# Kernel tuning notes

Measured on AMD Instinct MI355X. Metric: run time of the kernel, lower is better.

## Reference

```python
import jax, jax.numpy as jnp
import numpy as np

B, F, D, C, K = 131072, 32, 16, 64, 8  # batch, features, qsvt degree, classes, KAN grid
CLIP = 1.0 - 1e-6


def setup_inputs() -> dict:
    key = jax.random.key(0)
    ks = jax.random.split(key, 7)
    return {
        "X": jax.random.normal(ks[0], (B, F), jnp.float32),
        "qsvt_phases": 0.1 * jax.random.normal(ks[1], (D,), jnp.float32),
        "lcu_weights": jax.random.uniform(ks[2], (F, D), jnp.float32),
        "sum_scale": jnp.ones((F,), jnp.float32) + 0.1 * jax.random.normal(ks[3], (F,), jnp.float32),
        "sum_bias": 0.1 * jax.random.normal(ks[4], (F,), jnp.float32),
        "kan_coeff": jax.random.normal(ks[5], (C, F, K), jnp.float32) / np.sqrt(F * K),
        "kan_bias": jnp.zeros((C,), jnp.float32),
    }


def reference(X, qsvt_phases, lcu_weights, sum_scale, sum_bias, kan_coeff, kan_bias):
    # QSVT: Chebyshev-with-phases polynomial features of each scalar input,
    # vectorized over (batch, feature) instead of the original Python loops.
    degree = qsvt_phases.shape[0]
    grid = kan_coeff.shape[-1]
    theta = jnp.arccos(jnp.clip(X, -CLIP, CLIP))                  # [B,F]
    kd = jnp.arange(1, degree + 1, dtype=X.dtype)                 # [D]
    qsvt_vecs = jnp.cos(theta[..., None] * kd + qsvt_phases)      # [B,F,D]
    # LCU block: normalized linear combination over the degree axis -> scalar per (b,f)
    lcu = jnp.sum(qsvt_vecs * lcu_weights, axis=-1) / (
        jnp.sum(jnp.abs(lcu_weights), axis=-1) + 1e-6)            # [B,F]
    # QuantumSumBlock (one per feature): per-feature affine + tanh squash
    feat = jnp.tanh(sum_scale * lcu + sum_bias)                   # [B,F]
    # KAN layer: Chebyshev basis expansion then per-(class,feature,basis) coefficients
    t2 = jnp.arccos(jnp.clip(feat, -CLIP, CLIP))                  # [B,F]
    kk = jnp.arange(grid, dtype=X.dtype)                          # [K]
    basis = jnp.cos(t2[..., None] * kk)                           # [B,F,K]
    return jnp.einsum('bfk,cfk->bc', basis, kan_coeff) + kan_bias  # [B,C]
```

## Files before the change

### kernel.cpp

```cpp
#include <hip/hip_runtime.h>
#include <hip/hip_bf16.h>

#define F 32
#define Dd 16
#define C 64
#define Kk 8
#define CLIPV (1.0f - 1e-6f)
#define K2 2.8853900817779268f
#define NBLK 1024
#define MT 2

typedef short v8s __attribute__((ext_vector_type(8)));
typedef float v4f __attribute__((ext_vector_type(4)));
typedef float v2f __attribute__((ext_vector_type(2)));

static __device__ inline unsigned pkbf(float lo, float hi) {
    const unsigned l = __bfloat16_as_ushort(__float2bfloat16(lo));
    const unsigned hh = __bfloat16_as_ushort(__float2bfloat16(hi));
    return l | (hh << 16);
}

#define BAR_WRITES() do {                                        \
    asm volatile("s_waitcnt lgkmcnt(0)" ::: "memory");           \
    __builtin_amdgcn_s_barrier();                                \
    asm volatile("" ::: "memory");                               \
} while (0)
#define BAR_READS() do {                                         \
    asm volatile("" ::: "memory");                               \
    __builtin_amdgcn_s_barrier();                                \
    asm volatile("" ::: "memory");                               \
} while (0)

__global__ __launch_bounds__(256, 4) void qkan_kernel(
    const float* __restrict__ X,
    const float* __restrict__ phases,
    const float* __restrict__ lcu_w,
    const float* __restrict__ sscale,
    const float* __restrict__ sbias,
    const float* __restrict__ coeff,
    const float* __restrict__ kbias,
    float* __restrict__ out)
{
    __shared__ unsigned short s_basis[F * 512];

    const int tid = threadIdx.x;
    const int lane = tid & 63;
    const int wu = __builtin_amdgcn_readfirstlane(tid >> 6);
    const int h = lane >> 4;
    const int r16 = lane & 15;
    const int fe = tid & 31;
    const int fe7 = fe & 7;
    const int rg = tid >> 5;

    const int rb0 = blockIdx.x * (MT * 64);

    float xq[8];
    {
        const float* xp = X + (size_t)(rb0 + rg * 8) * F + fe;
#pragma unroll
        for (int m = 0; m < 8; ++m) xq[m] = __builtin_nontemporal_load(xp + m * F);
    }

    float sp0, cp0;
    __sincosf(phases[lane & 15], &sp0, &cp0);

    v2f cc[16];
    float fbias;
    {
        const float* lwf = lcu_w + fe * Dd;
        float wv[16];
        float asum = 0.f;
#pragma unroll
        for (int d = 0; d < Dd; ++d) {
            wv[d] = lwf[d];
            asum += fabsf(wv[d]);
        }
        const float sc = K2 * sscale[fe] / (asum + 1e-6f);
#pragma unroll
        for (int d = 0; d < Dd; ++d) {
            const float cpd = __shfl(cp0, d, 16);
            const float spd = __shfl(sp0, d, 16);
            cc[d][0] = sc * wv[d] * cpd;
            cc[d][1] = -sc * wv[d] * spd;
        }
        fbias = K2 * sbias[fe];
    }

    v8s Bfr[8];
    const int cidx = wu * 16 + r16;
#pragma unroll
    for (int q = 0; q < 8; ++q) {
        const float* gp = coeff + ((size_t)(cidx * F + 4 * q + h) * Kk);
        const float4 g0 = *reinterpret_cast<const float4*>(gp);
        const float4 g1 = *reinterpret_cast<const float4*>(gp + 4);
        union { unsigned u[4]; v8s v; } bb;
        bb.u[0] = pkbf(g0.x, g0.y);
        bb.u[1] = pkbf(g0.z, g0.w);
        bb.u[2] = pkbf(g1.x, g1.y);
        bb.u[3] = pkbf(g1.z, g1.w);
        Bfr[q] = bb.v;
    }
    const float biasreg = kbias[cidx];

    for (int mt = 0; mt < MT; ++mt) {
        const int row_base = rb0 + mt * 64;
        if (mt) BAR_READS();

        float xn[8];
        if (mt + 1 < MT) {
            const float* xp = X + (size_t)(row_base + 64 + rg * 8) * F + fe;
#pragma unroll
            for (int m = 0; m < 8; ++m) xn[m] = __builtin_nontemporal_load(xp + m * F);
        }

#pragma unroll
        for (int m = 0; m < 8; ++m) {
            const float x = __builtin_amdgcn_fmed3f(xq[m], -CLIPV, CLIPV);
            const float s1 = __builtin_amdgcn_sqrtf(__builtin_fmaf(-x, x, 1.f));
            const float tx = x + x;
            const v2f tx2 = {tx, tx};
            v2f w = {0.f, 0.f}, wp = {0.f, 0.f};
#pragma unroll
            for (int j = 15; j >= 0; --j) {
                const v2f wn = __builtin_elementwise_fma(tx2, w, cc[j] - wp);
                wp = w;
                w = wn;
            }
            float z = fbias - wp[0];
            z = __builtin_fmaf(x, w[0], z);
            z = __builtin_fmaf(s1, w[1], z);
            const float e = __builtin_amdgcn_exp2f(z);
            const float rr = __builtin_amdgcn_rcpf(e + 1.f);
            const float t = __builtin_fmaf(-2.f, rr, 1.f);
            const float t2 = t + t;
            const float b1 = t;
            const float b2 = t2 * b1 - 1.f;
            const float b3 = t2 * b2 - b1;
            const float b4 = t2 * b3 - b2;
            const float b5 = t2 * b4 - b3;
            const float b6 = t2 * b5 - b4;
            const float b7 = t2 * b6 - b5;
            uint4 pk;
            pk.x = pkbf(1.f, b1);
            pk.y = pkbf(b2, b3);
            pk.z = pkbf(b4, b5);
            pk.w = pkbf(b6, b7);
            *reinterpret_cast<uint4*>(
                &s_basis[fe * 512 + rg * 64 + ((m ^ fe7) << 3)]) = pk;
        }
        BAR_WRITES();

#pragma unroll
        for (int t = 0; t < 4; ++t) {
            const int s0 = ((t * 16 + r16) ^ h) << 3;
            v4f acc = {biasreg, biasreg, biasreg, biasreg};
#pragma unroll
            for (int q = 0; q < 8; ++q) {
                const int idx = (4 * q + h) * 512 + (s0 ^ ((q & 1) << 5));
                const v8s a = *reinterpret_cast<const v8s*>(&s_basis[idx]);
                acc = __builtin_amdgcn_mfma_f32_16x16x32_bf16(a, Bfr[q], acc, 0, 0, 0);
            }
            const int row0 = row_base + t * 16 + h * 4;
#pragma unroll
            for (int i = 0; i < 4; ++i) {
                __builtin_nontemporal_store(acc[i], &out[(size_t)(row0 + i) * C + cidx]);
            }
        }

        if (mt + 1 < MT) {
#pragma unroll
            for (int m = 0; m < 8; ++m) xq[m] = xn[m];
        }
    }
}

extern "C" void kernel_launch(void* const* d_in, const int* in_sizes, int n_in,
                              void* d_out, int out_size, void* d_ws, size_t ws_size,
                              hipStream_t stream) {
    const float* X  = (const float*)d_in[0];
    const float* ph = (const float*)d_in[1];
    const float* lw = (const float*)d_in[2];
    const float* ss = (const float*)d_in[3];
    const float* sb = (const float*)d_in[4];
    const float* kc = (const float*)d_in[5];
    const float* kb = (const float*)d_in[6];
    float* out = (float*)d_out;
    qkan_kernel<<<dim3(NBLK), dim3(256), 0, stream>>>(X, ph, lw, ss, sb, kc, kb, out);
}
```

Before: 24.81 us.

## Software-pipeline basis compute and MFMA with double-buffered LDS in 32-row stages

```diff
diff --git a/kernel.cpp b/kernel.cpp
--- a/kernel.cpp
+++ b/kernel.cpp
@@ -8,7 +8,7 @@
 #define CLIPV (1.0f - 1e-6f)
 #define K2 2.8853900817779268f
 #define NBLK 1024
-#define MT 2
+#define HALF 256
 
 typedef short v8s __attribute__((ext_vector_type(8)));
 typedef float v4f __attribute__((ext_vector_type(4)));
@@ -20,13 +20,8 @@
     return l | (hh << 16);
 }
 
-#define BAR_WRITES() do {                                        \
+#define BAR_LGKM() do {                                          \
     asm volatile("s_waitcnt lgkmcnt(0)" ::: "memory");           \
-    __builtin_amdgcn_s_barrier();                                \
-    asm volatile("" ::: "memory");                               \
-} while (0)
-#define BAR_READS() do {                                         \
-    asm volatile("" ::: "memory");                               \
     __builtin_amdgcn_s_barrier();                                \
     asm volatile("" ::: "memory");                               \
 } while (0)
@@ -41,7 +36,7 @@
     const float* __restrict__ kbias,
     float* __restrict__ out)
 {
-    __shared__ unsigned short s_basis[F * 512];
+    __shared__ unsigned short s_basis[2][F * HALF];
 
     const int tid = threadIdx.x;
     const int lane = tid & 63;
@@ -52,13 +47,13 @@
     const int fe7 = fe & 7;
     const int rg = tid >> 5;
 
-    const int rb0 = blockIdx.x * (MT * 64);
+    const int rb = blockIdx.x * 128;
 
-    float xq[8];
+    float xq[4], xn[4];
     {
-        const float* xp = X + (size_t)(rb0 + rg * 8) * F + fe;
+        const float* xp = X + (size_t)(rb + rg * 4) * F + fe;
 #pragma unroll
-        for (int m = 0; m < 8; ++m) xq[m] = __builtin_nontemporal_load(xp + m * F);
+        for (int m = 0; m < 4; ++m) xq[m] = __builtin_nontemporal_load(xp + m * F);
     }
 
     float sp0, cp0;
@@ -102,74 +97,80 @@
     }
     const float biasreg = kbias[cidx];
 
-    for (int mt = 0; mt < MT; ++mt) {
-        const int row_base = rb0 + mt * 64;
-        if (mt) BAR_READS();
-
-        float xn[8];
-        if (mt + 1 < MT) {
-            const float* xp = X + (size_t)(row_base + 64 + rg * 8) * F + fe;
 #pragma unroll
-            for (int m = 0; m < 8; ++m) xn[m] = __builtin_nontemporal_load(xp + m * F);
-        }
-
+    for (int s = 0; s < 5; ++s) {
+        if (s < 4) {
+            if (s + 1 < 4) {
+                const float* xp = X + (size_t)(rb + (s + 1) * 32 + rg * 4) * F + fe;
 #pragma unroll
-        for (int m = 0; m < 8; ++m) {
-            const float x = __builtin_amdgcn_fmed3f(xq[m], -CLIPV, CLIPV);
-            const float s1 = __builtin_amdgcn_sqrtf(__builtin_fmaf(-x, x, 1.f));
-            const float tx = x + x;
-            const v2f tx2 = {tx, tx};
-            v2f w = {0.f, 0.f}, wp = {0.f, 0.f};
+                for (int m = 0; m < 4; ++m)
+                    xn[m] = __builtin_nontemporal_load(xp + m * F);
+            }
+            unsigned short* buf = s_basis[s & 1];
 #pragma unroll
-            for (int j = 15; j >= 0; --j) {
-                const v2f wn = __builtin_elementwise_fma(tx2, w, cc[j] - wp);
-                wp = w;
-                w = wn;
-            }
-            float z = fbias - wp[0];
-            z = __builtin_fmaf(x, w[0], z);
-            z = __builtin_fmaf(s1, w[1], z);
-            const float e = __builtin_amdgcn_exp2f(z);
-            const float rr = __builtin_amdgcn_rcpf(e + 1.f);
-            const float t = __builtin_fmaf(-2.f, rr, 1.f);
-            const float t2 = t + t;
-            const float b1 = t;
-            const float b2 = t2 * b1 - 1.f;
-            const float b3 = t2 * b2 - b1;
-            const float b4 = t2 * b3 - b2;
-            const float b5 = t2 * b4 - b3;
-            const float b6 = t2 * b5 - b4;
-            const float b7 = t2 * b6 - b5;
-            uint4 pk;
-            pk.x = pkbf(1.f, b1);
-            pk.y = pkbf(b2, b3);
-            pk.z = pkbf(b4, b5);
-            pk.w = pkbf(b6, b7);
-            *reinterpret_cast<uint4*>(
-                &s_basis[fe * 512 + rg * 64 + ((m ^ fe7) << 3)]) = pk;
-        }
-        BAR_WRITES();
-
+            for (int m = 0; m < 4; ++m) {
+                const int row = rg * 4 + m;
+                const float x = __builtin_amdgcn_fmed3f(xq[m], -CLIPV, CLIPV);
+                const float s1 = __builtin_amdgcn_sqrtf(__builtin_fmaf(-x, x, 1.f));
+                const float tx = x + x;
+                const v2f tx2 = {tx, tx};
+                v2f w = {0.f, 0.f}, wp = {0.f, 0.f};
 #pragma unroll
-        for (int t = 0; t < 4; ++t) {
-            const int s0 = ((t * 16 + r16) ^ h) << 3;
-            v4f acc = {biasreg, biasreg, biasreg, biasreg};
-#pragma unroll
-            for (int q = 0; q < 8; ++q) {
-                const int idx = (4 * q + h) * 512 + (s0 ^ ((q & 1) << 5));
-                const v8s a = *reinterpret_cast<const v8s*>(&s_basis[idx]);
-                acc = __builtin_amdgcn_mfma_f32_16x16x32_bf16(a, Bfr[q], acc, 0, 0, 0);
-            }
-            const int row0 = row_base + t * 16 + h * 4;
-#pragma unroll
-            for (int i = 0; i < 4; ++i) {
-                __builtin_nontemporal_store(acc[i], &out[(size_t)(row0 + i) * C + cidx]);
+                for (int j = 15; j >= 0; --j) {
+                    const v2f wn = __builtin_elementwise_fma(tx2, w, cc[j] - wp);
+                    wp = w;
+                    w = wn;
+                }
+                float z = fbias - wp[0];
+                z = __builtin_fmaf(x, w[0], z);
+                z = __builtin_fmaf(s1, w[1], z);
+                const float e = __builtin_amdgcn_exp2f(z);
+                const float rr = __builtin_amdgcn_rcpf(e + 1.f);
+                const float t = __builtin_fmaf(-2.f, rr, 1.f);
+                const float t2 = t + t;
+                const float b1 = t;
+                const float b2 = t2 * b1 - 1.f;
+                const float b3 = t2 * b2 - b1;
+                const float b4 = t2 * b3 - b2;
+                const float b5 = t2 * b4 - b3;
+                const float b6 = t2 * b5 - b4;
+                const float b7 = t2 * b6 - b5;
+                uint4 pk;
+                pk.x = pkbf(1.f, b1);
+                pk.y = pkbf(b2, b3);
+                pk.z = pkbf(b4, b5);
+                pk.w = pkbf(b6, b7);
+                *reinterpret_cast<uint4*>(
+                    &buf[fe * HALF + ((row ^ fe7) << 3)]) = pk;
             }
         }
 
-        if (mt + 1 < MT) {
+        if (s >= 1) {
+            const unsigned short* buf = s_basis[(s - 1) & 1];
+            const int row_base = rb + (s - 1) * 32;
 #pragma unroll
-            for (int m = 0; m < 8; ++m) xq[m] = xn[m];
+            for (int t = 0; t < 2; ++t) {
+                const int s0 = ((t * 16 + r16) ^ h) << 3;
+                v4f acc = {biasreg, biasreg, biasreg, biasreg};
+#pragma unroll
+                for (int q = 0; q < 8; ++q) {
+                    const int idx = (4 * q + h) * HALF + (s0 ^ ((q & 1) << 5));
+                    const v8s a = *reinterpret_cast<const v8s*>(&buf[idx]);
+                    acc = __builtin_amdgcn_mfma_f32_16x16x32_bf16(a, Bfr[q], acc, 0, 0, 0);
+                }
+                const int row0 = row_base + t * 16 + h * 4;
+#pragma unroll
+                for (int i = 0; i < 4; ++i) {
+                    __builtin_nontemporal_store(
+                        acc[i], &out[(size_t)(row0 + i) * C + cidx]);
+                }
+            }
+        }
+
+        if (s < 4) {
+            BAR_LGKM();
+#pragma unroll
+            for (int m = 0; m < 4; ++m) xq[m] = xn[m];
         }
     }
 }
```

After: 30.02 us. 1.21x slower.
